# Kernel optimization log

Hardware: AMD Instinct MI355X
Metric: run time of the kernel (lower is better)

## Reference

```python
import jax, jax.numpy as jnp
import numpy as np


def _mlp(x, W1, b1, W2, b2):
    # x: (B, M, T); torch MLPLayer: transpose(1,2) -> Linear -> Linear -> LeakyReLU -> transpose back
    h = jnp.einsum('bmt,hm->bht', x, W1) + b1[None, :, None]   # (B, H, T)
    y = jnp.einsum('bht,oh->bot', h, W2) + b2[None, :, None]   # (B, M, T)
    return jax.nn.leaky_relu(y, negative_slope=0.01)


def _calc_attn(q, k, v):
    # q: (B, M, Tq), k: (B, M, Tk), v: (B, M, Tk)
    Tq = q.shape[-1]
    qk = jnp.einsum('bmq,bmk->bqk', q, k)                       # (B, Tq, Tk)
    eye = jnp.eye(Tq, dtype=qk.dtype)                           # broadcasts: (Tq,Tq) or (1,1)
    logits = jnp.exp(qk - qk * eye / jnp.sqrt(jnp.asarray(Tq, qk.dtype)))
    scores = jax.nn.softmax(logits, axis=-1)
    return jnp.einsum('bqk,bmk->bmq', scores, v)                # (B, M, Tq)


def setup_inputs() -> dict:
    key = jax.random.key(0)
    B, M, T, H = 16, 128, 2048, 512
    ks = jax.random.split(key, 14)
    s = 0.02
    inp = {
        'pattern': jax.random.normal(ks[0], (B, M, T), jnp.float32),
        'value': jax.random.normal(ks[1], (B, M, T), jnp.float32),
        'kernel_size': 33,
    }
    names = ['q', 'k', 'o']
    for i, n in enumerate(names):
        inp['W%s1' % n] = jax.random.normal(ks[2 + 4 * i], (H, M), jnp.float32) * s
        inp['b%s1' % n] = jax.random.normal(ks[3 + 4 * i], (H,), jnp.float32) * s
        inp['W%s2' % n] = jax.random.normal(ks[4 + 4 * i], (M, H), jnp.float32) * s
        inp['b%s2' % n] = jax.random.normal(ks[5 + 4 * i], (M,), jnp.float32) * s
    return inp


def reference(pattern, value, kernel_size, Wq1, bq1, Wq2, bq2, Wk1, bk1, Wk2, bk2, Wo1, bo1, Wo2, bo2):
    query = _mlp(pattern, Wq1, bq1, Wq2, bq2)
    key = _mlp(pattern, Wk1, bk1, Wk2, bk2)
    # full (internal) attention
    attn_in = _calc_attn(query, key, value)                     # (B, M, T)
    rep_in = _mlp(attn_in, Wo1, bo1, Wo2, bo2)
    # windowed (external) attention
    T = query.shape[-1]
    cu = (kernel_size - 1) // 2
    q_w = query[..., T - 1 - cu : T - cu]                       # (B, M, 1)
    k_w = key[..., kernel_size - cu - 1 : T - cu - 2]           # (B, M, T-k-1)
    v_w = value[..., kernel_size : T - 1]                       # (B, M, T-k-1)
    attn_ex = _calc_attn(q_w, k_w, v_w)                         # (B, M, 1)
    rep_ex = _mlp(attn_ex, Wo1, bo1, Wo2, bo2)
    return jnp.concatenate([rep_in, rep_ex], axis=-1)           # (B, M, T+1)
```

## Files before the change

kernel.cpp:

```cpp
#include <hip/hip_runtime.h>
#include <hip/hip_bf16.h>
#include <math.h>

#define B_    16
#define M_    128
#define T_    2048
#define H_    512
#define TOUT_ 2049

typedef unsigned short u16;
typedef unsigned int   u32;
typedef __bf16 bf16x8 __attribute__((ext_vector_type(8)));
typedef float  f32x16 __attribute__((ext_vector_type(16)));
typedef float  f32x4  __attribute__((ext_vector_type(4)));
typedef u32    u32x4  __attribute__((ext_vector_type(4)));
typedef u32    u32x2  __attribute__((ext_vector_type(2)));

#define A_OFF     0
#define C_OFF     16384
#define MEAN_OFF  16896
#define AQKBF_OFF 19200
#define AOBF_OFF  35584
#define QT_OFF    43776
#define KT_OFF    (43776 + 2097152)
#define VB_OFF    (43776 + 2 * 2097152)

static __device__ __forceinline__ u16 f2bf(float f) {
  u32 u = __float_as_uint(f);
  u = (u + 0x7FFFu + ((u >> 16) & 1u)) >> 16;
  return (u16)u;
}
static __device__ __forceinline__ u32 pk2(float lo, float hi) {
  __hip_bfloat162 h = __float22bfloat162_rn(float2{lo, hi});
  u32 r;
  __builtin_memcpy(&r, &h, 4);
  return r;
}
static __device__ __forceinline__ bf16x8 ldfrag(const u16* p) {
  return __builtin_bit_cast(bf16x8, *(const u32x4*)p);
}
static __device__ __forceinline__ float ex2(float x) {
#if __has_builtin(__builtin_amdgcn_exp2f)
  return __builtin_amdgcn_exp2f(x);
#else
  return exp2f(x);
#endif
}

__global__ __launch_bounds__(128) void fuse_weights_all(
    const float* __restrict__ W1q, const float* __restrict__ b1q,
    const float* __restrict__ W2q, const float* __restrict__ b2q,
    const float* __restrict__ W1k, const float* __restrict__ b1k,
    const float* __restrict__ W2k, const float* __restrict__ b2k,
    const float* __restrict__ W1o, const float* __restrict__ b1o,
    const float* __restrict__ W2o, const float* __restrict__ b2o,
    float* __restrict__ A, float* __restrict__ c,
    u16* __restrict__ Aqk_bf, u16* __restrict__ Ao_bf) {
  __shared__ float w2row[H_];
  int which = blockIdx.x >> 7;
  int o = blockIdx.x & 127;
  const float* W1 = which == 0 ? W1q : which == 1 ? W1k : W1o;
  const float* b1 = which == 0 ? b1q : which == 1 ? b1k : b1o;
  const float* W2 = which == 0 ? W2q : which == 1 ? W2k : W2o;
  const float* b2 = which == 0 ? b2q : which == 1 ? b2k : b2o;
  int m = threadIdx.x;
  for (int h = m; h < H_; h += 128) w2row[h] = W2[o * H_ + h];
  __syncthreads();
  float acc = 0.f;
#pragma unroll 8
  for (int h = 0; h < H_; ++h) acc = fmaf(w2row[h], W1[h * M_ + m], acc);
  u16 ab = f2bf(acc);
  if (which == 0)      Aqk_bf[o * 128 + m] = ab;
  else if (which == 1) Aqk_bf[(128 + o) * 128 + m] = ab;
  else               { Ao_bf[o * 128 + m] = ab; A[o * M_ + m] = acc; }
  if (m < 64) {
    float cc = 0.f;
    for (int h = m; h < H_; h += 64) cc = fmaf(w2row[h], b1[h], cc);
#pragma unroll
    for (int off = 32; off > 0; off >>= 1) cc += __shfl_down(cc, off, 64);
    if (m == 0) c[which * 128 + o] = cc + b2[o];
  }
}

#define XS 68

__global__ __launch_bounds__(256) void prep_kernel(
    const float* __restrict__ pattern, const u16* __restrict__ Aqk_bf,
    const float* __restrict__ cqk, u16* __restrict__ qT, u16* __restrict__ kT,
    const float* __restrict__ value, u16* __restrict__ vb,
    float* __restrict__ meanv) {
  __shared__ alignas(16) float xsf[128 * XS];
  int bx = blockIdx.x;
  int tid = threadIdx.x;

  if (bx >= 512) {
    int bm = bx - 512;
    float* red = xsf;
    const float* row = value + (size_t)bm * T_;
    int i0 = tid * 8;
    float4 a = *(const float4*)(row + i0);
    float4 bq = *(const float4*)(row + i0 + 4);
    u32x4 o = {pk2(a.x, a.y), pk2(a.z, a.w), pk2(bq.x, bq.y), pk2(bq.z, bq.w)};
    *(u32x4*)&vb[(size_t)bm * T_ + i0] = o;
    float vals[8] = {a.x, a.y, a.z, a.w, bq.x, bq.y, bq.z, bq.w};
    float s = 0.f;
#pragma unroll
    for (int j = 0; j < 8; ++j) {
      int idx = i0 + j;
      if (idx >= 33 && idx < T_ - 1) s += vals[j];
    }
    red[tid] = s;
    __syncthreads();
    for (int st = 128; st > 0; st >>= 1) {
      if (tid < st) red[tid] += red[tid + st];
      __syncthreads();
    }
    if (tid == 0) meanv[bm] = red[0] * (1.f / 2014.f);
    return;
  }

  int b = bx >> 5;
  int t0 = (bx & 31) * 64;
  int lane = tid & 63;
  int wv = tid >> 6;
  int l31 = lane & 31;
  int lh8 = (lane >> 5) * 8;

  bf16x8 afr[2][8];
#pragma unroll
  for (int i = 0; i < 2; ++i) {
    const u16* ap = Aqk_bf + ((2 * wv + i) * 32 + l31) * 128 + lh8;
#pragma unroll
    for (int s = 0; s < 8; ++s) afr[i][s] = ldfrag(ap + 16 * s);
  }

#pragma unroll
  for (int rep = 0; rep < 8; ++rep) {
    int m = rep * 16 + (tid >> 4);
    int tc = (tid & 15) * 4;
    float4 v = *(const float4*)&pattern[(size_t)(b * M_ + m) * T_ + t0 + tc];
    *(float4*)&xsf[m * XS + tc] = v;
  }
  __syncthreads();

  bf16x8 bfr[2][8];
#pragma unroll
  for (int tt = 0; tt < 2; ++tt) {
#pragma unroll
    for (int s = 0; s < 8; ++s) {
      float v0 = xsf[(s * 16 + lh8 + 0) * XS + tt * 32 + l31];
      float v1 = xsf[(s * 16 + lh8 + 1) * XS + tt * 32 + l31];
      float v2 = xsf[(s * 16 + lh8 + 2) * XS + tt * 32 + l31];
      float v3 = xsf[(s * 16 + lh8 + 3) * XS + tt * 32 + l31];
      float v4 = xsf[(s * 16 + lh8 + 4) * XS + tt * 32 + l31];
      float v5 = xsf[(s * 16 + lh8 + 5) * XS + tt * 32 + l31];
      float v6 = xsf[(s * 16 + lh8 + 6) * XS + tt * 32 + l31];
      float v7 = xsf[(s * 16 + lh8 + 7) * XS + tt * 32 + l31];
      u32x4 p = {pk2(v0, v1), pk2(v2, v3), pk2(v4, v5), pk2(v6, v7)};
      bfr[tt][s] = __builtin_bit_cast(bf16x8, p);
    }
  }
  __syncthreads();

  u16* obuf = (u16*)xsf;
#pragma unroll
  for (int tt = 0; tt < 2; ++tt) {
#pragma unroll
    for (int i = 0; i < 2; ++i) {
      f32x16 acc;
#pragma unroll
      for (int r = 0; r < 16; ++r) acc[r] = 0.f;
#pragma unroll
      for (int s = 0; s < 8; ++s)
        acc = __builtin_amdgcn_mfma_f32_32x32x16_bf16(afr[i][s], bfr[tt][s], acc, 0, 0, 0);
      int ot = 2 * wv + i;
      int t = tt * 32 + l31;
      float sc = (ot < 4) ? 1.44269504f : 1.0f;
#pragma unroll
      for (int r = 0; r < 16; ++r) {
        int orow = (r & 3) + 8 * (r >> 2) + 4 * (lane >> 5);
        float v = acc[r] + cqk[ot * 32 + orow];
        v = v > 0.f ? v : 0.01f * v;
        obuf[t * 258 + ot * 32 + orow] = f2bf(v * sc);
      }
    }
  }
  __syncthreads();

  const u32* ob32 = (const u32*)obuf;
#pragma unroll
  for (int g = 0; g < 8; ++g) {
    int G = wv * 8 + g;
    int mat = G >> 4;
    int t = (G & 15) * 4 + (lane >> 4);
    int og2 = lane & 15;
    int wbase = t * 129 + mat * 64 + og2 * 4;
    u32x4 vv = {ob32[wbase], ob32[wbase + 1], ob32[wbase + 2], ob32[wbase + 3]};
    u32* dst = (u32*)((mat ? kT : qT) + ((size_t)(b * T_ + t0 + t)) * 128) + og2 * 4;
    *(u32x4*)dst = vv;
  }
}

#define QSTR 136
#define VSTR 72
#define KTILE 64
#define NKT  (T_ / KTILE)
#define CINIT 0.52876637f

__global__ __launch_bounds__(1024, 4) void attn_mfma_kernel(
    const u16* __restrict__ qT, const u16* __restrict__ kT,
    const u16* __restrict__ vB, const u16* __restrict__ Ao_bf,
    const float* __restrict__ co, const float* __restrict__ Aofp,
    const float* __restrict__ meanv, float* __restrict__ out) {
  extern __shared__ u16 smem[];
  u16* ks0 = smem;
  u16* ks1 = smem + 8704;
  u16* vs0 = smem + 17408;
  u16* vs1 = smem + 26624;
  float* pbuf  = (float*)smem;
  u16*   ptbuf = smem + 33024;
  float* dls   = (float*)(smem + 50432);

  int b = blockIdx.y;
  int q0 = blockIdx.x * 128;
  int tid = threadIdx.x;
  int lane = tid & 63;
  int wv = tid >> 6;
  int l31 = lane & 31;
  int h = lane >> 5;
  int lh8 = h * 8;
  int qt = wv & 3;
  int kh = (wv >> 2) & 1;
  int mh = wv >> 3;

  const u16* gkb = kT + (size_t)b * T_ * 128;
  const u16* gvb = vB + (size_t)b * M_ * T_;
  int kr = tid >> 4, kc = (tid & 15) * 8;
  int vr = tid >> 3, vc = (tid & 7) * 8;

  bf16x8 qfrag[8];
  {
    const u16* qrow = qT + (size_t)(b * T_ + q0 + qt * 32 + l31) * 128 + lh8;
#pragma unroll
    for (int s = 0; s < 8; ++s) qfrag[s] = ldfrag(qrow + s * 16);
  }

  u32x4 kreg, vreg;
  kreg = *(const u32x4*)&gkb[(size_t)kr * 128 + kc];
  vreg = *(const u32x4*)&gvb[(size_t)vr * T_ + vc];
  *(u32x4*)&ks0[kr * QSTR + kc] = kreg;
  *(u32x4*)&vs0[vr * VSTR + vc] = vreg;
  kreg = *(const u32x4*)&gkb[(size_t)(KTILE + kr) * 128 + kc];
  vreg = *(const u32x4*)&gvb[(size_t)vr * T_ + KTILE + vc];

  f32x16 pacc[2];
  float den = 0.f;
#pragma unroll
  for (int i = 0; i < 16; ++i) { pacc[0][i] = 0.f; pacc[1][i] = 0.f; }

  for (int kt = 0; kt < NKT; ++kt) {
    u16* kcur = (kt & 1) ? ks1 : ks0;
    u16* knxt = (kt & 1) ? ks0 : ks1;
    u16* vcur = (kt & 1) ? vs1 : vs0;
    u16* vnxt = (kt & 1) ? vs0 : vs1;
    __syncthreads();

    if (kt < NKT - 1) {
      *(u32x4*)&knxt[kr * QSTR + kc] = kreg;
      *(u32x4*)&vnxt[vr * VSTR + vc] = vreg;
      int kn = (kt + 2 < NKT) ? (kt + 2) * KTILE : (NKT - 1) * KTILE;
      kreg = *(const u32x4*)&gkb[(size_t)(kn + kr) * 128 + kc];
      vreg = *(const u32x4*)&gvb[(size_t)vr * T_ + kn + vc];
    }

    f32x16 sacc;
#pragma unroll
    for (int i = 0; i < 16; ++i) sacc[i] = CINIT;
    {
      const u16* krow = &kcur[(kh * 32 + l31) * QSTR + lh8];
#pragma unroll
      for (int s = 0; s < 8; ++s) {
        bf16x8 kf = ldfrag(krow + s * 16);
        sacc = __builtin_amdgcn_mfma_f32_32x32x16_bf16(kf, qfrag[s], sacc, 0, 0, 0);
      }
    }

    if (kt * KTILE + kh * 32 == q0 + qt * 32) {
#pragma unroll
      for (int r = 0; r < 16; ++r) {
        int row = (r & 3) + 8 * (r >> 2) + 4 * h;
        if (row == l31) sacc[r] = fmaf(sacc[r], 0.97790291f, 0.01168420f);
      }
    }

    float w[16];
#pragma unroll
    for (int r = 0; r < 16; ++r) w[r] = ex2(ex2(sacc[r]));
    {
      float d0 = (w[0] + w[1]) + (w[2] + w[3]);
      float d1 = (w[4] + w[5]) + (w[6] + w[7]);
      float d2 = (w[8] + w[9]) + (w[10] + w[11]);
      float d3 = (w[12] + w[13]) + (w[14] + w[15]);
      den += (d0 + d1) + (d2 + d3);
    }
    u32 p00 = pk2(w[0], w[1]),  p01 = pk2(w[2], w[3]);
    u32 p10 = pk2(w[4], w[5]),  p11 = pk2(w[6], w[7]);
    u32 p20 = pk2(w[8], w[9]),  p21 = pk2(w[10], w[11]);
    u32 p30 = pk2(w[12], w[13]), p31 = pk2(w[14], w[15]);
    u32 e0 = __shfl_xor(h ? p00 : p10, 32, 64);
    u32 e1 = __shfl_xor(h ? p01 : p11, 32, 64);
    u32 e2 = __shfl_xor(h ? p20 : p30, 32, 64);
    u32 e3 = __shfl_xor(h ? p21 : p31, 32, 64);
    u32x4 f0 = h ? u32x4{e0, e1, p10, p11} : u32x4{p00, p01, e0, e1};
    u32x4 f1 = h ? u32x4{e2, e3, p30, p31} : u32x4{p20, p21, e2, e3};
    bf16x8 bw0 = __builtin_bit_cast(bf16x8, f0);
    bf16x8 bw1 = __builtin_bit_cast(bf16x8, f1);

#pragma unroll
    for (int i = 0; i < 2; ++i) {
      int mtg = mh * 2 + i;
      const u16* vrow = &vcur[(mtg * 32 + l31) * VSTR + kh * 32 + lh8];
      bf16x8 vf0 = ldfrag(vrow);
      bf16x8 vf1 = ldfrag(vrow + 16);
      pacc[i] = __builtin_amdgcn_mfma_f32_32x32x16_bf16(vf0, bw0, pacc[i], 0, 0, 0);
      pacc[i] = __builtin_amdgcn_mfma_f32_32x32x16_bf16(vf1, bw1, pacc[i], 0, 0, 0);
    }
  }

  float dq = den + __shfl_xor(den, 32, 64);

  __syncthreads();

  if (kh == 1) {
#pragma unroll
    for (int i = 0; i < 2; ++i) {
      float* pb = &pbuf[(((qt * 2 + mh) * 2 + i) * 64 + lane) * 16];
#pragma unroll
      for (int g = 0; g < 4; ++g) {
        f32x4 v = {pacc[i][4 * g], pacc[i][4 * g + 1],
                   pacc[i][4 * g + 2], pacc[i][4 * g + 3]};
        *(f32x4*)(pb + 4 * g) = v;
      }
    }
    if (mh == 0 && lane < 32) dls[qt * 32 + lane] = dq;
  }
  __syncthreads();

  if (kh == 0) {
    float rden = 1.f / (dq + dls[qt * 32 + l31]);
#pragma unroll
    for (int i = 0; i < 2; ++i) {
      const float* pb = &pbuf[(((qt * 2 + mh) * 2 + i) * 64 + lane) * 16];
#pragma unroll
      for (int g = 0; g < 4; ++g) {
        f32x4 t = *(const f32x4*)(pb + 4 * g);
        float v0 = (pacc[i][4 * g + 0] + t[0]) * rden;
        float v1 = (pacc[i][4 * g + 1] + t[1]) * rden;
        float v2 = (pacc[i][4 * g + 2] + t[2]) * rden;
        float v3 = (pacc[i][4 * g + 3] + t[3]) * rden;
        int m0 = (mh * 2 + i) * 32 + 8 * g + 4 * h;
        u32x2 wp = {pk2(v0, v1), pk2(v2, v3)};
        *(u32x2*)&ptbuf[(qt * 32 + l31) * QSTR + m0] = wp;
      }
    }
  }
  __syncthreads();

  bf16x8 aofr[8];
  {
    const u16* ap = Ao_bf + ((wv & 3) * 32 + l31) * 128 + lh8;
#pragma unroll
    for (int s = 0; s < 8; ++s) aofr[s] = ldfrag(ap + 16 * s);
  }
  {
    int qt2 = wv >> 2;
    bf16x8 pfr[8];
    const u16* pp = &ptbuf[(qt2 * 32 + l31) * QSTR + lh8];
#pragma unroll
    for (int s = 0; s < 8; ++s) pfr[s] = ldfrag(pp + 16 * s);
    f32x16 oacc;
#pragma unroll
    for (int r = 0; r < 16; ++r) oacc[r] = 0.f;
#pragma unroll
    for (int s = 0; s < 8; ++s)
      oacc = __builtin_amdgcn_mfma_f32_32x32x16_bf16(aofr[s], pfr[s], oacc, 0, 0, 0);
#pragma unroll
    for (int r = 0; r < 16; ++r) {
      int orow = (wv & 3) * 32 + (r & 3) + 8 * (r >> 2) + 4 * h;
      float v = oacc[r] + co[orow];
      v = v > 0.f ? v : 0.01f * v;
      out[((size_t)(b * M_ + orow)) * TOUT_ + q0 + qt2 * 32 + l31] = v;
    }
  }

  if (blockIdx.x == 0 && tid < 128) {
    float acc = co[tid];
    const float* mv = meanv + b * 128;
    for (int m = 0; m < 128; ++m) acc = fmaf(Aofp[tid * 128 + m], mv[m], acc);
    acc = acc > 0.f ? acc : 0.01f * acc;
    out[((size_t)(b * M_ + tid)) * TOUT_ + 2048] = acc;
  }
}

extern "C" void kernel_launch(void* const* d_in, const int* in_sizes, int n_in,
                              void* d_out, int out_size, void* d_ws, size_t ws_size,
                              hipStream_t stream) {
  (void)in_sizes; (void)n_in; (void)out_size; (void)ws_size;
  const float* pattern = (const float*)d_in[0];
  const float* value   = (const float*)d_in[1];
  const float* Wq1 = (const float*)d_in[3];
  const float* bq1 = (const float*)d_in[4];
  const float* Wq2 = (const float*)d_in[5];
  const float* bq2 = (const float*)d_in[6];
  const float* Wk1 = (const float*)d_in[7];
  const float* bk1 = (const float*)d_in[8];
  const float* Wk2 = (const float*)d_in[9];
  const float* bk2 = (const float*)d_in[10];
  const float* Wo1 = (const float*)d_in[11];
  const float* bo1 = (const float*)d_in[12];
  const float* Wo2 = (const float*)d_in[13];
  const float* bo2 = (const float*)d_in[14];

  float* ws     = (float*)d_ws;
  float* A      = ws + A_OFF;
  float* c      = ws + C_OFF;
  float* meanv  = ws + MEAN_OFF;
  u16*   Aqk_bf = (u16*)(ws + AQKBF_OFF);
  u16*   Ao_bf  = (u16*)(ws + AOBF_OFF);
  u16*   qT     = (u16*)(ws + QT_OFF);
  u16*   kT     = (u16*)(ws + KT_OFF);
  u16*   vB     = (u16*)(ws + VB_OFF);
  float* out    = (float*)d_out;

  fuse_weights_all<<<384, 128, 0, stream>>>(
      Wq1, bq1, Wq2, bq2, Wk1, bk1, Wk2, bk2, Wo1, bo1, Wo2, bo2,
      A, c, Aqk_bf, Ao_bf);

  prep_kernel<<<512 + B_ * M_, 256, 0, stream>>>(
      pattern, Aqk_bf, c, qT, kT, value, vB, meanv);

  size_t lds_bytes = 101376;
  attn_mfma_kernel<<<dim3(T_ / 128, B_), 1024, lds_bytes, stream>>>(
      qT, kT, vB, Ao_bf, c + 256, A, meanv, out);
}
```

Measured before the change: 210.2 us.

## Split attention warps into QK/softmax producers and loader waves with LDS-staged probabilities

Restructures the attention loop so waves 0-7 compute QK scores and exponentials and write bf16 probabilities into shared memory. Waves 8-15 prefetch the next K/V tile from global memory, and then all 16 waves run the PV MFMAs, each owning one 32-row M slice. This removes the cross-half shuffle and the post-loop partial-accumulator reduction, and shrinks LDS use. In exchange it adds a second barrier per tile and leaves half the waves idle during the score phase, which may serialize work that used to overlap.

```diff
diff --git a/kernel.cpp b/kernel.cpp
--- a/kernel.cpp
+++ b/kernel.cpp
@@ -203,6 +203,8 @@
 
 #define QSTR 136
 #define VSTR 72
+#define PSTR 72
+#define PTSTR 136
 #define KTILE 64
 #define NKT  (T_ / KTILE)
 #define CINIT 0.52876637f
@@ -217,9 +219,9 @@
   u16* ks1 = smem + 8704;
   u16* vs0 = smem + 17408;
   u16* vs1 = smem + 26624;
-  float* pbuf  = (float*)smem;
-  u16*   ptbuf = smem + 33024;
-  float* dls   = (float*)(smem + 50432);
+  u16* pls = smem + 35840;
+  float* dls   = (float*)smem;
+  u16*   ptbuf = smem + 17408;
 
   int b = blockIdx.y;
   int q0 = blockIdx.x * 128;
@@ -230,33 +232,32 @@
   int h = lane >> 5;
   int lh8 = h * 8;
   int qt = wv & 3;
-  int kh = (wv >> 2) & 1;
-  int mh = wv >> 3;
+  int ksl = wv >> 2;
+  int mt = wv >> 2;
 
   const u16* gkb = kT + (size_t)b * T_ * 128;
   const u16* gvb = vB + (size_t)b * M_ * T_;
-  int kr = tid >> 4, kc = (tid & 15) * 8;
-  int vr = tid >> 3, vc = (tid & 7) * 8;
 
   bf16x8 qfrag[8];
+  if (wv < 8) {
+    const u16* qrow = qT + (size_t)(b * T_ + q0 + qt * 32 + l31) * 128 + lh8;
+#pragma unroll
+    for (int s = 0; s < 8; ++s) qfrag[s] = ldfrag(qrow + s * 16);
+  }
+
   {
-    const u16* qrow = qT + (size_t)(b * T_ + q0 + qt * 32 + l31) * 128 + lh8;
-#pragma unroll
-    for (int s = 0; s < 8; ++s) qfrag[s] = ldfrag(qrow + s * 16);
-  }
-
-  u32x4 kreg, vreg;
-  kreg = *(const u32x4*)&gkb[(size_t)kr * 128 + kc];
-  vreg = *(const u32x4*)&gvb[(size_t)vr * T_ + vc];
-  *(u32x4*)&ks0[kr * QSTR + kc] = kreg;
-  *(u32x4*)&vs0[vr * VSTR + vc] = vreg;
-  kreg = *(const u32x4*)&gkb[(size_t)(KTILE + kr) * 128 + kc];
-  vreg = *(const u32x4*)&gvb[(size_t)vr * T_ + KTILE + vc];
-
-  f32x16 pacc[2];
+    int kr = tid >> 4, kc = (tid & 15) * 8;
+    int vr = tid >> 3, vc = (tid & 7) * 8;
+    *(u32x4*)&ks0[kr * QSTR + kc] = *(const u32x4*)&gkb[(size_t)kr * 128 + kc];
+    *(u32x4*)&vs0[vr * VSTR + vc] = *(const u32x4*)&gvb[(size_t)vr * T_ + vc];
+  }
+
+  f32x16 pacc;
   float den = 0.f;
 #pragma unroll
-  for (int i = 0; i < 16; ++i) { pacc[0][i] = 0.f; pacc[1][i] = 0.f; }
+  for (int i = 0; i < 16; ++i) pacc[i] = 0.f;
+
+  int t9 = tid & 511;
 
   for (int kt = 0; kt < NKT; ++kt) {
     u16* kcur = (kt & 1) ? ks1 : ks0;
@@ -265,103 +266,88 @@
     u16* vnxt = (kt & 1) ? vs0 : vs1;
     __syncthreads();
 
-    if (kt < NKT - 1) {
-      *(u32x4*)&knxt[kr * QSTR + kc] = kreg;
-      *(u32x4*)&vnxt[vr * VSTR + vc] = vreg;
-      int kn = (kt + 2 < NKT) ? (kt + 2) * KTILE : (NKT - 1) * KTILE;
-      kreg = *(const u32x4*)&gkb[(size_t)(kn + kr) * 128 + kc];
-      vreg = *(const u32x4*)&gvb[(size_t)vr * T_ + kn + vc];
-    }
-
-    f32x16 sacc;
-#pragma unroll
-    for (int i = 0; i < 16; ++i) sacc[i] = CINIT;
+    u32x4 kr0, kr1, vr0, vr1;
+    if (wv < 8) {
+      f32x16 sacc;
+#pragma unroll
+      for (int i = 0; i < 16; ++i) sacc[i] = CINIT;
+      {
+        const u16* krow = &kcur[(ksl * 32 + l31) * QSTR + lh8];
+#pragma unroll
+        for (int s = 0; s < 8; ++s) {
+          bf16x8 kf = ldfrag(krow + s * 16);
+          sacc = __builtin_amdgcn_mfma_f32_32x32x16_bf16(kf, qfrag[s], sacc, 0, 0, 0);
+        }
+      }
+      if (kt * KTILE + ksl * 32 == q0 + qt * 32) {
+#pragma unroll
+        for (int r = 0; r < 16; ++r) {
+          int row = (r & 3) + 8 * (r >> 2) + 4 * h;
+          if (row == l31) sacc[r] = fmaf(sacc[r], 0.97790291f, 0.01168420f);
+        }
+      }
+      float w[16];
+#pragma unroll
+      for (int r = 0; r < 16; ++r) w[r] = ex2(ex2(sacc[r]));
+      {
+        float d0 = (w[0] + w[1]) + (w[2] + w[3]);
+        float d1 = (w[4] + w[5]) + (w[6] + w[7]);
+        float d2 = (w[8] + w[9]) + (w[10] + w[11]);
+        float d3 = (w[12] + w[13]) + (w[14] + w[15]);
+        den += (d0 + d1) + (d2 + d3);
+      }
+      u16* prow = &pls[(qt * 32 + l31) * PSTR + ksl * 32 + 4 * h];
+#pragma unroll
+      for (int g = 0; g < 4; ++g) {
+        u32x2 wp = {pk2(w[4 * g], w[4 * g + 1]), pk2(w[4 * g + 2], w[4 * g + 3])};
+        *(u32x2*)&prow[8 * g] = wp;
+      }
+    } else if (kt < NKT - 1) {
+      int kn = (kt + 1) * KTILE;
+      int ka0 = t9 >> 4, kb0 = (t9 & 15) * 8;
+      int va0 = t9 >> 3, vb0 = (t9 & 7) * 8;
+      kr0 = *(const u32x4*)&gkb[(size_t)(kn + ka0) * 128 + kb0];
+      kr1 = *(const u32x4*)&gkb[(size_t)(kn + ka0 + 32) * 128 + kb0];
+      vr0 = *(const u32x4*)&gvb[(size_t)va0 * T_ + kn + vb0];
+      vr1 = *(const u32x4*)&gvb[(size_t)(va0 + 64) * T_ + kn + vb0];
+    }
+
+    __syncthreads();
+
     {
-      const u16* krow = &kcur[(kh * 32 + l31) * QSTR + lh8];
-#pragma unroll
-      for (int s = 0; s < 8; ++s) {
-        bf16x8 kf = ldfrag(krow + s * 16);
-        sacc = __builtin_amdgcn_mfma_f32_32x32x16_bf16(kf, qfrag[s], sacc, 0, 0, 0);
-      }
-    }
-
-    if (kt * KTILE + kh * 32 == q0 + qt * 32) {
-#pragma unroll
-      for (int r = 0; r < 16; ++r) {
-        int row = (r & 3) + 8 * (r >> 2) + 4 * h;
-        if (row == l31) sacc[r] = fmaf(sacc[r], 0.97790291f, 0.01168420f);
-      }
-    }
-
-    float w[16];
-#pragma unroll
-    for (int r = 0; r < 16; ++r) w[r] = ex2(ex2(sacc[r]));
-    {
-      float d0 = (w[0] + w[1]) + (w[2] + w[3]);
-      float d1 = (w[4] + w[5]) + (w[6] + w[7]);
-      float d2 = (w[8] + w[9]) + (w[10] + w[11]);
-      float d3 = (w[12] + w[13]) + (w[14] + w[15]);
-      den += (d0 + d1) + (d2 + d3);
-    }
-    u32 p00 = pk2(w[0], w[1]),  p01 = pk2(w[2], w[3]);
-    u32 p10 = pk2(w[4], w[5]),  p11 = pk2(w[6], w[7]);
-    u32 p20 = pk2(w[8], w[9]),  p21 = pk2(w[10], w[11]);
-    u32 p30 = pk2(w[12], w[13]), p31 = pk2(w[14], w[15]);
-    u32 e0 = __shfl_xor(h ? p00 : p10, 32, 64);
-    u32 e1 = __shfl_xor(h ? p01 : p11, 32, 64);
-    u32 e2 = __shfl_xor(h ? p20 : p30, 32, 64);
-    u32 e3 = __shfl_xor(h ? p21 : p31, 32, 64);
-    u32x4 f0 = h ? u32x4{e0, e1, p10, p11} : u32x4{p00, p01, e0, e1};
-    u32x4 f1 = h ? u32x4{e2, e3, p30, p31} : u32x4{p20, p21, e2, e3};
-    bf16x8 bw0 = __builtin_bit_cast(bf16x8, f0);
-    bf16x8 bw1 = __builtin_bit_cast(bf16x8, f1);
-
-#pragma unroll
-    for (int i = 0; i < 2; ++i) {
-      int mtg = mh * 2 + i;
-      const u16* vrow = &vcur[(mtg * 32 + l31) * VSTR + kh * 32 + lh8];
-      bf16x8 vf0 = ldfrag(vrow);
-      bf16x8 vf1 = ldfrag(vrow + 16);
-      pacc[i] = __builtin_amdgcn_mfma_f32_32x32x16_bf16(vf0, bw0, pacc[i], 0, 0, 0);
-      pacc[i] = __builtin_amdgcn_mfma_f32_32x32x16_bf16(vf1, bw1, pacc[i], 0, 0, 0);
-    }
-  }
-
+      const u16* vrow = &vcur[(mt * 32 + l31) * VSTR + lh8];
+      const u16* prow = &pls[(qt * 32 + l31) * PSTR + lh8];
+#pragma unroll
+      for (int k16 = 0; k16 < 4; ++k16) {
+        bf16x8 vf = ldfrag(vrow + k16 * 16);
+        bf16x8 pf = ldfrag(prow + k16 * 16);
+        pacc = __builtin_amdgcn_mfma_f32_32x32x16_bf16(vf, pf, pacc, 0, 0, 0);
+      }
+    }
+
+    if (wv >= 8 && kt < NKT - 1) {
+      int ka0 = t9 >> 4, kb0 = (t9 & 15) * 8;
+      int va0 = t9 >> 3, vb0 = (t9 & 7) * 8;
+      *(u32x4*)&knxt[ka0 * QSTR + kb0] = kr0;
+      *(u32x4*)&knxt[(ka0 + 32) * QSTR + kb0] = kr1;
+      *(u32x4*)&vnxt[va0 * VSTR + vb0] = vr0;
+      *(u32x4*)&vnxt[(va0 + 64) * VSTR + vb0] = vr1;
+    }
+  }
+
+  __syncthreads();
   float dq = den + __shfl_xor(den, 32, 64);
-
-  __syncthreads();
-
-  if (kh == 1) {
-#pragma unroll
-    for (int i = 0; i < 2; ++i) {
-      float* pb = &pbuf[(((qt * 2 + mh) * 2 + i) * 64 + lane) * 16];
-#pragma unroll
-      for (int g = 0; g < 4; ++g) {
-        f32x4 v = {pacc[i][4 * g], pacc[i][4 * g + 1],
-                   pacc[i][4 * g + 2], pacc[i][4 * g + 3]};
-        *(f32x4*)(pb + 4 * g) = v;
-      }
-    }
-    if (mh == 0 && lane < 32) dls[qt * 32 + lane] = dq;
-  }
-  __syncthreads();
-
-  if (kh == 0) {
-    float rden = 1.f / (dq + dls[qt * 32 + l31]);
-#pragma unroll
-    for (int i = 0; i < 2; ++i) {
-      const float* pb = &pbuf[(((qt * 2 + mh) * 2 + i) * 64 + lane) * 16];
-#pragma unroll
-      for (int g = 0; g < 4; ++g) {
-        f32x4 t = *(const f32x4*)(pb + 4 * g);
-        float v0 = (pacc[i][4 * g + 0] + t[0]) * rden;
-        float v1 = (pacc[i][4 * g + 1] + t[1]) * rden;
-        float v2 = (pacc[i][4 * g + 2] + t[2]) * rden;
-        float v3 = (pacc[i][4 * g + 3] + t[3]) * rden;
-        int m0 = (mh * 2 + i) * 32 + 8 * g + 4 * h;
-        u32x2 wp = {pk2(v0, v1), pk2(v2, v3)};
-        *(u32x2*)&ptbuf[(qt * 32 + l31) * QSTR + m0] = wp;
-      }
+  if (wv < 8 && lane < 32) dls[ksl * 128 + qt * 32 + l31] = dq;
+  __syncthreads();
+
+  {
+    float rden = 1.f / (dls[qt * 32 + l31] + dls[128 + qt * 32 + l31]);
+    u16* pt = &ptbuf[(qt * 32 + l31) * PTSTR + mt * 32 + 4 * h];
+#pragma unroll
+    for (int g = 0; g < 4; ++g) {
+      u32x2 wp = {pk2(pacc[4 * g] * rden, pacc[4 * g + 1] * rden),
+                  pk2(pacc[4 * g + 2] * rden, pacc[4 * g + 3] * rden)};
+      *(u32x2*)&pt[8 * g] = wp;
     }
   }
   __syncthreads();
@@ -375,7 +361,7 @@
   {
     int qt2 = wv >> 2;
     bf16x8 pfr[8];
-    const u16* pp = &ptbuf[(qt2 * 32 + l31) * QSTR + lh8];
+    const u16* pp = &ptbuf[(qt2 * 32 + l31) * PTSTR + lh8];
 #pragma unroll
     for (int s = 0; s < 8; ++s) pfr[s] = ldfrag(pp + 16 * s);
     f32x16 oacc;
@@ -439,7 +425,7 @@
   prep_kernel<<<512 + B_ * M_, 256, 0, stream>>>(
       pattern, Aqk_bf, c, qT, kT, value, vB, meanv);
 
-  size_t lds_bytes = 101376;
+  size_t lds_bytes = 90112;
   attn_mfma_kernel<<<dim3(T_ / 128, B_), 1024, lds_bytes, stream>>>(
       qT, kT, vB, Ao_bf, c + 256, A, meanv, out);
 }
```

New measurement: 195.3 us. 7.1% less time.
